# Optimization experiments

Measured on AMD Instinct MI355X. Metric: run time of the kernel, lower is better.

Reference implementation:

```python
import jax, jax.numpy as jnp
import numpy as np

N = 50000
E = 800000
DIM = 256
H = 8
HD = DIM // H


def setup_inputs() -> dict:
    key = jax.random.key(0)
    ks = jax.random.split(key, 8)
    s = 0.02
    return {
        "x": jax.random.normal(ks[0], (N, DIM), jnp.float32),
        "src": jax.random.randint(ks[1], (E,), 0, N, jnp.int32),
        "dst": jax.random.randint(ks[2], (E,), 0, N, jnp.int32),
        "Wqkv": jax.random.normal(ks[3], (DIM, 3 * DIM), jnp.float32) * s,
        "bqkv": jnp.zeros((3 * DIM,), jnp.float32),
        "Wout": jax.random.normal(ks[4], (DIM, DIM), jnp.float32) * s,
        "bout": jnp.zeros((DIM,), jnp.float32),
        "W1": jax.random.normal(ks[5], (2 * DIM, DIM), jnpp := jnp.float32) * s,
        "b1": jnp.zeros((DIM,), jnp.float32),
        "W2": jax.random.normal(ks[6], (DIM, DIM), jnp.float32) * s,
        "b2": jnp.zeros((DIM,), jnp.float32),
    }


def reference(x, src, dst, Wqkv, bqkv, Wout, bout, W1, b1, W2, b2):
    n = x.shape[0]
    scale = 1.0 / np.sqrt(HD).astype(np.float32)
    # QKV projection; torch reshapes [N, 3*dim] -> [N, H, 3*hd] then splits per head
    qkv = (x @ Wqkv + bqkv).reshape(n, H, 3 * HD)
    q, k, v = qkv[..., :HD], qkv[..., HD:2 * HD], qkv[..., 2 * HD:]
    # per-edge attention scores: key at src dotted with query at dst -> [E, H]
    scores = jnp.einsum('ehd,ehd->eh', k[src], q[dst]) * scale
    # edge softmax grouped by destination node
    m = jax.ops.segment_max(scores, dst, num_segments=n)  # [N, H]
    p = jnp.exp(scores - m[dst])
    denom = jax.ops.segment_sum(p, dst, num_segments=n)  # [N, H]
    probs = p / denom[dst]
    # weighted scatter-sum aggregation of source values -> [N, H, HD]
    agg = jax.ops.segment_sum(v[src] * probs[..., None], dst, num_segments=n)
    agg = agg.reshape(n, DIM) @ Wout + bout
    # feed-forward over concat([x, aggregated])
    h = jnp.concatenate([x, agg], axis=1)
    h = jax.nn.gelu(h @ W1 + b1, approximate=False)
    return h @ W2 + b2
```

## Files before the change

kernel.cpp:

```cpp
#include <hip/hip_runtime.h>
#include <hip/hip_bf16.h>
#include <math.h>

#define NDIM 256
#define HDIM 32
#define SCB 512

typedef __attribute__((ext_vector_type(8))) short bf16x8;
typedef __attribute__((ext_vector_type(4))) float f32x4;
typedef __attribute__((ext_vector_type(2))) float f32x2;
typedef unsigned long long ull;

__device__ inline float bf2f(unsigned short u) {
  union { unsigned int i; float f; } c; c.i = ((unsigned int)u) << 16; return c.f;
}
__device__ inline unsigned short f2bf(float f) {
  union { float f; unsigned int i; } c; c.f = f;
  unsigned int x = c.i;
  unsigned int lsb = (x >> 16) & 1u;
  x += 0x7fffu + lsb;
  return (unsigned short)(x >> 16);
}
__device__ inline float4 ldbf4(const unsigned short* p) {
  ull raw = *(const ull*)p;
  float4 f;
  f.x = bf2f((unsigned short)(raw));
  f.y = bf2f((unsigned short)(raw >> 16));
  f.z = bf2f((unsigned short)(raw >> 32));
  f.w = bf2f((unsigned short)(raw >> 48));
  return f;
}
__device__ inline void stbf4(unsigned short* p, float4 v) {
  ull raw = (ull)f2bf(v.x) | ((ull)f2bf(v.y) << 16)
          | ((ull)f2bf(v.z) << 32) | ((ull)f2bf(v.w) << 48);
  *(ull*)p = raw;
}
__device__ inline ull pk4_bf16(float v0, float v1, float v2, float v3) {
  return (ull)f2bf(v0) | ((ull)f2bf(v1) << 16) | ((ull)f2bf(v2) << 32) | ((ull)f2bf(v3) << 48);
}

__device__ inline unsigned char f2e4m3(float v) {
#if __has_builtin(__builtin_amdgcn_cvt_pk_fp8_f32)
  return (unsigned char)(__builtin_amdgcn_cvt_pk_fp8_f32(v, v, 0, false) & 0xff);
#else
  union { float f; unsigned int u; } c; c.f = v;
  unsigned char s = (unsigned char)((c.u >> 24) & 0x80);
  float a = fabsf(v);
  if (!(a < 448.f)) return (unsigned char)(s | 0x7e);
  if (a < 0.0009765625f) return s;
  int e = (int)((c.u >> 23) & 0xff) - 127;
  if (e < -6) {
    int q = (int)rintf(ldexpf(a, 9));
    if (q >= 8) return (unsigned char)(s | 0x08);
    return (unsigned char)(s | q);
  }
  int q = (int)rintf(ldexpf(a, 3 - e));
  if (q == 16) { e++; q = 8; }
  if (e > 8) return (unsigned char)(s | 0x7e);
  return (unsigned char)(s | ((e + 7) << 3) | (q - 8));
#endif
}
__device__ inline unsigned int pk4_e4m3(float v0, float v1, float v2, float v3) {
#if __has_builtin(__builtin_amdgcn_cvt_pk_fp8_f32)
  int w = __builtin_amdgcn_cvt_pk_fp8_f32(v0, v1, 0, false);
  w = __builtin_amdgcn_cvt_pk_fp8_f32(v2, v3, w, true);
  return (unsigned int)w;
#else
  return (unsigned int)f2e4m3(v0) | ((unsigned int)f2e4m3(v1) << 8)
       | ((unsigned int)f2e4m3(v2) << 16) | ((unsigned int)f2e4m3(v3) << 24);
#endif
}
template<bool HI>
__device__ inline f32x2 e4m3pk(unsigned int w) {
#if __has_builtin(__builtin_amdgcn_cvt_pk_f32_fp8)
  return __builtin_amdgcn_cvt_pk_f32_fp8((int)w, HI);
#else
  unsigned int h = HI ? (w >> 16) : w;
  f32x2 r;
  #pragma unroll
  for (int j = 0; j < 2; ++j) {
    unsigned char b = (unsigned char)(h >> (8 * j));
    int e = (b >> 3) & 0xf, mm = b & 7;
    float val = e ? ldexpf((float)(8 + mm), e - 10) : ldexpf((float)mm, -9);
    r[j] = (b & 0x80) ? -val : val;
  }
  return r;
#endif
}

__global__ void fuse0_k(
    const float* __restrict__ x, unsigned short* __restrict__ xb, int n8, int nbx,
    const float* __restrict__ Wqkv, unsigned short* __restrict__ wqkvt,
    const float* __restrict__ W1, unsigned short* __restrict__ wf,
    const float* __restrict__ W2, unsigned short* __restrict__ w2t,
    const float* __restrict__ Wout, const float* __restrict__ bout,
    const float* __restrict__ b1, float* __restrict__ bc, int nbw,
    const int* __restrict__ dst, int* __restrict__ deg, int E)
{
  int b = blockIdx.x;
  int tid = threadIdx.x;
  if (b < nbx) {
    int i = b * 256 + tid;
    if (i < n8) {
      const float* p = x + (size_t)i * 8;
      float4 a = *(const float4*)p;
      float4 bv = *(const float4*)(p + 4);
      ull lo = (ull)f2bf(a.x) | ((ull)f2bf(a.y) << 16) | ((ull)f2bf(a.z) << 32) | ((ull)f2bf(a.w) << 48);
      ull hi = (ull)f2bf(bv.x) | ((ull)f2bf(bv.y) << 16) | ((ull)f2bf(bv.z) << 32) | ((ull)f2bf(bv.w) << 48);
      ull* d = (ull*)(xb + (size_t)i * 8);
      d[0] = lo; d[1] = hi;
    }
    return;
  }
  b -= nbx;
  if (b < nbw) {
    int idx = b * 256 + tid;
    if (idx < 196608) {
      int j = idx >> 8, k = idx & 255;
      int seg = j >> 8, jj = j & 255;
      int h = jj >> 5, t = jj & 31;
      int orig = h * 96 + seg * 32 + t;
      wqkvt[(size_t)j * 256 + k] = f2bf(Wqkv[(size_t)k * 768 + orig]);
    } else if (idx < 262144) {
      int i2 = idx - 196608;
      int n = i2 >> 8, k = i2 & 255;
      wf[(size_t)n * 512 + k] = f2bf(W1[(size_t)k * 256 + n]);
    } else if (idx < 327680) {
      int i3 = idx - 262144;
      int n = i3 >> 8, k = i3 & 255;
      w2t[(size_t)n * 256 + k] = f2bf(W2[(size_t)k * 256 + n]);
    } else if (idx < 393216) {
      int i4 = idx - 327680;
      int a = i4 >> 8, n = i4 & 255;
      float s = 0.f;
      #pragma unroll 4
      for (int j = 0; j < 256; ++j)
        s += Wout[(size_t)a * 256 + j] * W1[(size_t)(256 + j) * 256 + n];
      wf[(size_t)n * 512 + 256 + a] = f2bf(s);
    } else if (idx < 393472) {
      int n = idx - 393216;
      float s = b1[n];
      for (int j = 0; j < 256; ++j)
        s += bout[j] * W1[(size_t)(256 + j) * 256 + n];
      bc[n] = s;
    }
    return;
  }
  b -= nbw;
  int e = b * 256 + tid;
  if (e < E) atomicAdd(&deg[dst[e]], 1);
}

__global__ __launch_bounds__(SCB) void bsum_k(const int* __restrict__ deg, int* __restrict__ bsum, int n) {
  int tid = threadIdx.x;
  int i = blockIdx.x * SCB + tid;
  int v = (i < n) ? deg[i] : 0;
  #pragma unroll
  for (int d = 1; d < 64; d <<= 1) v += __shfl_xor(v, d);
  __shared__ int wsum[8];
  if ((tid & 63) == 0) wsum[tid >> 6] = v;
  __syncthreads();
  if (tid == 0) {
    int s = 0;
    #pragma unroll
    for (int j = 0; j < 8; ++j) s += wsum[j];
    bsum[blockIdx.x] = s;
  }
}

__global__ __launch_bounds__(128) void bscan_k(int* __restrict__ bsum, int nb) {
  __shared__ int tmp[128];
  int tid = threadIdx.x;
  int v = (tid < nb) ? bsum[tid] : 0;
  tmp[tid] = v;
  __syncthreads();
  for (int d = 1; d < 128; d <<= 1) {
    int t = (tid >= d) ? tmp[tid - d] : 0;
    __syncthreads();
    tmp[tid] += t;
    __syncthreads();
  }
  if (tid < nb) bsum[tid] = tmp[tid];
}

__global__ __launch_bounds__(SCB) void offs_k(const int* __restrict__ deg, const int* __restrict__ bsum,
                                              int* __restrict__ offs, int* __restrict__ cursor, int n) {
  int tid = threadIdx.x, lane = tid & 63, wid = tid >> 6;
  int b = blockIdx.x;
  int i = b * SCB + tid;
  int v = (i < n) ? deg[i] : 0;
  int incl = v;
  #pragma unroll
  for (int d = 1; d < 64; d <<= 1) { int t = __shfl_up(incl, d); if (lane >= d) incl += t; }
  __shared__ int wsum[8];
  if (lane == 63) wsum[wid] = incl;
  __syncthreads();
  if (tid < 8) {
    int s = wsum[tid];
    #pragma unroll
    for (int d = 1; d < 8; d <<= 1) { int t = __shfl_up(s, d); if (tid >= d) s += t; }
    wsum[tid] = s;
  }
  __syncthreads();
  int base = (b > 0 ? bsum[b - 1] : 0) + (wid > 0 ? wsum[wid - 1] : 0);
  if (i < n) {
    int val = base + incl - v;
    offs[i] = val;
    cursor[i] = val;
  }
  if (i == n - 1) offs[n] = base + incl;
}

__global__ __launch_bounds__(256) void attn_k(
    const unsigned short* Q,
    const unsigned char* __restrict__ K8,
    const unsigned char* __restrict__ V8,
    const int* __restrict__ offs,
    const int* __restrict__ ssrc,
    unsigned short* agg, int N)
{
  int n = blockIdx.x * 4 + (threadIdx.x >> 6);
  if (n >= N) return;
  int lane = threadIdx.x & 63;
  int col = lane << 2;
  const float scale = 0.17677669529663689f;
  float4 q4 = ldbf4(Q + (size_t)n * NDIM + col);
  q4.x *= scale; q4.y *= scale; q4.z *= scale; q4.w *= scale;
  int e0 = offs[n], e1 = offs[n + 1];
  float den = 0.f;
  float ax = 0.f, ay = 0.f, az = 0.f, aw = 0.f;
  int e = e0;
  for (; e + 8 <= e1; e += 8) {
    unsigned int kw[8], vw[8];
    #pragma unroll
    for (int j = 0; j < 8; ++j) {
      int s = ssrc[e + j];
      kw[j] = *(const unsigned int*)(K8 + (size_t)s * NDIM + col);
      vw[j] = *(const unsigned int*)(V8 + (size_t)s * NDIM + col);
    }
    float d[8];
    #pragma unroll
    for (int j = 0; j < 8; ++j) {
      f32x2 k01 = e4m3pk<false>(kw[j]);
      f32x2 k23 = e4m3pk<true>(kw[j]);
      d[j] = q4.x * k01[0] + q4.y * k01[1] + q4.z * k23[0] + q4.w * k23[1];
    }
    #pragma unroll
    for (int j = 0; j < 8; ++j) {
      d[j] += __shfl_xor(d[j], 1);
      d[j] += __shfl_xor(d[j], 2);
      d[j] += __shfl_xor(d[j], 4);
    }
    #pragma unroll
    for (int j = 0; j < 8; ++j) {
      float p = __expf(d[j]);
      den += p;
      f32x2 v01 = e4m3pk<false>(vw[j]);
      f32x2 v23 = e4m3pk<true>(vw[j]);
      ax += p * v01[0]; ay += p * v01[1];
      az += p * v23[0]; aw += p * v23[1];
    }
  }
  for (; e + 4 <= e1; e += 4) {
    unsigned int kw[4], vw[4];
    #pragma unroll
    for (int j = 0; j < 4; ++j) {
      int s = ssrc[e + j];
      kw[j] = *(const unsigned int*)(K8 + (size_t)s * NDIM + col);
      vw[j] = *(const unsigned int*)(V8 + (size_t)s * NDIM + col);
    }
    float d[4];
    #pragma unroll
    for (int j = 0; j < 4; ++j) {
      f32x2 k01 = e4m3pk<false>(kw[j]);
      f32x2 k23 = e4m3pk<true>(kw[j]);
      d[j] = q4.x * k01[0] + q4.y * k01[1] + q4.z * k23[0] + q4.w * k23[1];
    }
    #pragma unroll
    for (int j = 0; j < 4; ++j) {
      d[j] += __shfl_xor(d[j], 1);
      d[j] += __shfl_xor(d[j], 2);
      d[j] += __shfl_xor(d[j], 4);
    }
    #pragma unroll
    for (int j = 0; j < 4; ++j) {
      float p = __expf(d[j]);
      den += p;
      f32x2 v01 = e4m3pk<false>(vw[j]);
      f32x2 v23 = e4m3pk<true>(vw[j]);
      ax += p * v01[0]; ay += p * v01[1];
      az += p * v23[0]; aw += p * v23[1];
    }
  }
  for (; e < e1; ++e) {
    int s = ssrc[e];
    unsigned int kw = *(const unsigned int*)(K8 + (size_t)s * NDIM + col);
    unsigned int vw = *(const unsigned int*)(V8 + (size_t)s * NDIM + col);
    f32x2 k01 = e4m3pk<false>(kw);
    f32x2 k23 = e4m3pk<true>(kw);
    float d = q4.x * k01[0] + q4.y * k01[1] + q4.z * k23[0] + q4.w * k23[1];
    d += __shfl_xor(d, 1);
    d += __shfl_xor(d, 2);
    d += __shfl_xor(d, 4);
    float p = __expf(d);
    den += p;
    f32x2 v01 = e4m3pk<false>(vw);
    f32x2 v23 = e4m3pk<true>(vw);
    ax += p * v01[0]; ay += p * v01[1];
    az += p * v23[0]; aw += p * v23[1];
  }
  float inv = (den > 0.f) ? 1.f / den : 0.f;
  stbf4(agg + (size_t)n * NDIM + col, make_float4(ax * inv, ay * inv, az * inv, aw * inv));
}

__global__ __launch_bounds__(256, 4) void sqkv_k(
    const int* __restrict__ src, const int* __restrict__ dstv,
    int* __restrict__ cursor, int* __restrict__ ssrc, int E, int nsc,
    const unsigned short* __restrict__ A1, const unsigned short* __restrict__ Wt,
    const float* __restrict__ bias,
    unsigned short* __restrict__ Oq, unsigned char* __restrict__ Ok, unsigned char* __restrict__ Ov,
    int M)
{
  __shared__ char smem[32768];
  if (blockIdx.x < nsc) {
    int e = blockIdx.x * 256 + threadIdx.x;
    if (e < E) {
      int p = atomicAdd(&cursor[dstv[e]], 1);
      ssrc[p] = src[e];
    }
    return;
  }
  unsigned short* As = (unsigned short*)smem;
  unsigned short* Bs = (unsigned short*)(smem + 16384);
  const int tid = threadIdx.x;
  const int lane = tid & 63;
  const int wid = tid >> 6;

  const int nwg = gridDim.x - nsc;
  const int bid = blockIdx.x - nsc;
  const int q8 = nwg >> 3, r8 = nwg & 7;
  const int xcd = bid & 7, idx8 = bid >> 3;
  const int swz = (xcd < r8 ? xcd * (q8 + 1) : r8 * (q8 + 1) + (xcd - r8) * q8) + idx8;
  const int nct = 6;
  const int bmt = swz / nct;
  const int bnt = swz - bmt * nct;
  const int bm = bmt * 128;
  const int bn = bnt * 128;

  const int wr = (wid >> 1) << 6;
  const int wc = (wid & 1) << 6;
  const int l15 = lane & 15, lhi = lane >> 4;
  const int srow = lane >> 3;
  const int ssl = (((lane & 7) ^ (lane >> 3)) << 3);

  f32x4 acc[4][4];
  #pragma unroll
  for (int i = 0; i < 4; ++i)
    #pragma unroll
    for (int j = 0; j < 4; ++j) acc[i][j] = (f32x4){0.f, 0.f, 0.f, 0.f};

  for (int k0 = 0; k0 < 256; k0 += 64) {
    #pragma unroll
    for (int t = 0; t < 4; ++t) {
      int qi = wid * 4 + t;
      const unsigned short* ga = A1 + (size_t)(bm + qi * 8 + srow) * 256 + k0 + ssl;
      __builtin_amdgcn_global_load_lds(
          (const __attribute__((address_space(1))) void*)ga,
          (__attribute__((address_space(3))) void*)&As[qi * 512], 16, 0, 0);
      const unsigned short* gb = Wt + (size_t)(bn + qi * 8 + srow) * 256 + k0 + ssl;
      __builtin_amdgcn_global_load_lds(
          (const __attribute__((address_space(1))) void*)gb,
          (__attribute__((address_space(3))) void*)&Bs[qi * 512], 16, 0, 0);
    }
    __syncthreads();
    #pragma unroll
    for (int kk = 0; kk < 64; kk += 32) {
      bf16x8 af[4], bfr[4];
      #pragma unroll
      for (int mi = 0; mi < 4; ++mi) {
        int rA = wr + mi * 16 + l15;
        af[mi] = *(const bf16x8*)&As[rA * 64 + ((((kk >> 3) + lhi) ^ (rA & 7)) << 3)];
      }
      #pragma unroll
      for (int ni = 0; ni < 4; ++ni) {
        int rB = wc + ni * 16 + l15;
        bfr[ni] = *(const bf16x8*)&Bs[rB * 64 + ((((kk >> 3) + lhi) ^ (rB & 7)) << 3)];
      }
      #pragma unroll
      for (int mi = 0; mi < 4; ++mi)
        #pragma unroll
        for (int ni = 0; ni < 4; ++ni)
          acc[mi][ni] = __builtin_amdgcn_mfma_f32_16x16x32_bf16(bfr[ni], af[mi], acc[mi][ni], 0, 0, 0);
    }
    __syncthreads();
  }

  const int seg = (bn + wc) >> 8;
  const int jjbase = (bn + wc) & 255;
  if (seg == 0) {
    unsigned short* slab = (unsigned short*)(smem + wid * 8192);
    #pragma unroll
    for (int ni = 0; ni < 4; ++ni) {
      int cl = ni * 16 + (lhi << 2);
      int jj = jjbase + cl;
      float4 bb = *(const float4*)&bias[(jj >> 5) * 96 + (jj & 31)];
      #pragma unroll
      for (int mi = 0; mi < 4; ++mi) {
        int rl = mi * 16 + l15;
        *(ull*)&slab[rl * 64 + cl] = pk4_bf16(
            acc[mi][ni][0] + bb.x, acc[mi][ni][1] + bb.y,
            acc[mi][ni][2] + bb.z, acc[mi][ni][3] + bb.w);
      }
    }
    asm volatile("s_waitcnt lgkmcnt(0)" ::: "memory");
    __builtin_amdgcn_sched_barrier(0);
    int rl0 = lane >> 3, coff = (lane & 7) << 3;
    #pragma unroll
    for (int t = 0; t < 8; ++t) {
      int rl = t * 8 + rl0;
      int gr = bm + wr + rl;
      if (gr < M)
        *(float4*)&Oq[(size_t)gr * NDIM + jjbase + coff] = *(float4*)&slab[rl * 64 + coff];
    }
  } else {
    unsigned char* slab8 = (unsigned char*)(smem + wid * 8192);
    unsigned char* dstp = (seg == 1) ? Ok : Ov;
    #pragma unroll
    for (int ni = 0; ni < 4; ++ni) {
      int cl = ni * 16 + (lhi << 2);
      int jj = jjbase + cl;
      float4 bb = *(const float4*)&bias[(jj >> 5) * 96 + seg * 32 + (jj & 31)];
      #pragma unroll
      for (int mi = 0; mi < 4; ++mi) {
        int rl = mi * 16 + l15;
        *(unsigned int*)&slab8[rl * 64 + cl] = pk4_e4m3(
            acc[mi][ni][0] + bb.x, acc[mi][ni][1] + bb.y,
            acc[mi][ni][2] + bb.z, acc[mi][ni][3] + bb.w);
      }
    }
    asm volatile("s_waitcnt lgkmcnt(0)" ::: "memory");
    __builtin_amdgcn_sched_barrier(0);
    int rl0 = lane >> 2, coff = (lane & 3) << 4;
    #pragma unroll
    for (int t = 0; t < 4; ++t) {
      int rl = t * 16 + rl0;
      int gr = bm + wr + rl;
      if (gr < M)
        *(float4*)&dstp[(size_t)gr * NDIM + jjbase + coff] = *(float4*)&slab8[rl * 64 + coff];
    }
  }
}

template<int EPI>
__global__ __launch_bounds__(256, 4) void mgemm_k(
    const unsigned short* __restrict__ A1, const unsigned short* __restrict__ A2,
    const unsigned short* __restrict__ Wt, const float* __restrict__ bias,
    float* __restrict__ Cf, unsigned short* __restrict__ Cb,
    int M, int K1, int K, int Ncol, int ldb, int nct)
{
  __shared__ char smem[32768];
  unsigned short* As = (unsigned short*)smem;
  unsigned short* Bs = (unsigned short*)(smem + 16384);
  const int tid = threadIdx.x;
  const int lane = tid & 63;
  const int wid = tid >> 6;

  const int nwg = gridDim.x;
  const int q8 = nwg >> 3, r8 = nwg & 7;
  const int xcd = blockIdx.x & 7, idx8 = blockIdx.x >> 3;
  const int swz = (xcd < r8 ? xcd * (q8 + 1) : r8 * (q8 + 1) + (xcd - r8) * q8) + idx8;
  const int bmt = swz / nct;
  const int bnt = swz - bmt * nct;
  const int bm = bmt * 128;
  const int bn = bnt * 128;

  const int wr = (wid >> 1) << 6;
  const int wc = (wid & 1) << 6;
  const int l15 = lane & 15, lhi = lane >> 4;
  const int srow = lane >> 3;
  const int ssl = (((lane & 7) ^ (lane >> 3)) << 3);

  f32x4 acc[4][4];
  #pragma unroll
  for (int i = 0; i < 4; ++i)
    #pragma unroll
    for (int j = 0; j < 4; ++j) acc[i][j] = (f32x4){0.f, 0.f, 0.f, 0.f};

  for (int k0 = 0; k0 < K; k0 += 64) {
    const unsigned short* Ab;
    int ks;
    if (k0 < K1) { Ab = A1; ks = k0; } else { Ab = A2; ks = k0 - K1; }
    #pragma unroll
    for (int t = 0; t < 4; ++t) {
      int qi = wid * 4 + t;
      const unsigned short* ga = Ab + (size_t)(bm + qi * 8 + srow) * 256 + ks + ssl;
      __builtin_amdgcn_global_load_lds(
          (const __attribute__((address_space(1))) void*)ga,
          (__attribute__((address_space(3))) void*)&As[qi * 512], 16, 0, 0);
      const unsigned short* gb = Wt + (size_t)(bn + qi * 8 + srow) * ldb + k0 + ssl;
      __builtin_amdgcn_global_load_lds(
          (const __attribute__((address_space(1))) void*)gb,
          (__attribute__((address_space(3))) void*)&Bs[qi * 512], 16, 0, 0);
    }
    __syncthreads();
    #pragma unroll
    for (int kk = 0; kk < 64; kk += 32) {
      bf16x8 af[4], bfr[4];
      #pragma unroll
      for (int mi = 0; mi < 4; ++mi) {
        int rA = wr + mi * 16 + l15;
        af[mi] = *(const bf16x8*)&As[rA * 64 + ((((kk >> 3) + lhi) ^ (rA & 7)) << 3)];
      }
      #pragma unroll
      for (int ni = 0; ni < 4; ++ni) {
        int rB = wc + ni * 16 + l15;
        bfr[ni] = *(const bf16x8*)&Bs[rB * 64 + ((((kk >> 3) + lhi) ^ (rB & 7)) << 3)];
      }
      #pragma unroll
      for (int mi = 0; mi < 4; ++mi)
        #pragma unroll
        for (int ni = 0; ni < 4; ++ni)
          acc[mi][ni] = __builtin_amdgcn_mfma_f32_16x16x32_bf16(bfr[ni], af[mi], acc[mi][ni], 0, 0, 0);
    }
    __syncthreads();
  }

  if (EPI == 0) {
    float* slabf = (float*)(smem + wid * 8192);
    #pragma unroll
    for (int half = 0; half < 2; ++half) {
      #pragma unroll
      for (int nj = 0; nj < 2; ++nj) {
        int ni = half * 2 + nj;
        int cl = nj * 16 + (lhi << 2);
        float4 bb = *(const float4*)&bias[bn + wc + half * 32 + cl];
        #pragma unroll
        for (int mi = 0; mi < 4; ++mi) {
          int rl = mi * 16 + l15;
          *(float4*)&slabf[rl * 32 + cl] = make_float4(
              acc[mi][ni][0] + bb.x, acc[mi][ni][1] + bb.y,
              acc[mi][ni][2] + bb.z, acc[mi][ni][3] + bb.w);
        }
      }
      asm volatile("s_waitcnt lgkmcnt(0)" ::: "memory");
      __builtin_amdgcn_sched_barrier(0);
      int rl0 = lane >> 3, coff = (lane & 7) << 2;
      #pragma unroll
      for (int t = 0; t < 8; ++t) {
        int rl = t * 8 + rl0;
        int gr = bm + wr + rl;
        if (gr < M)
          *(float4*)&Cf[(size_t)gr * Ncol + bn + wc + half * 32 + coff] =
              *(float4*)&slabf[rl * 32 + coff];
      }
      if (half == 0) {
        asm volatile("s_waitcnt lgkmcnt(0)" ::: "memory");
        __builtin_amdgcn_sched_barrier(0);
      }
    }
  } else {
    unsigned short* slab = (unsigned short*)(smem + wid * 8192);
    #pragma unroll
    for (int ni = 0; ni < 4; ++ni) {
      int cl = ni * 16 + (lhi << 2);
      float4 bb = *(const float4*)&bias[bn + wc + cl];
      #pragma unroll
      for (int mi = 0; mi < 4; ++mi) {
        int rl = mi * 16 + l15;
        float v0 = acc[mi][ni][0] + bb.x;
        float v1 = acc[mi][ni][1] + bb.y;
        float v2 = acc[mi][ni][2] + bb.z;
        float v3 = acc[mi][ni][3] + bb.w;
        v0 = 0.5f * v0 * (1.0f + erff(v0 * 0.70710678118654752f));
        v1 = 0.5f * v1 * (1.0f + erff(v1 * 0.70710678118654752f));
        v2 = 0.5f * v2 * (1.0f + erff(v2 * 0.70710678118654752f));
        v3 = 0.5f * v3 * (1.0f + erff(v3 * 0.70710678118654752f));
        *(ull*)&slab[rl * 64 + cl] = pk4_bf16(v0, v1, v2, v3);
      }
    }
    asm volatile("s_waitcnt lgkmcnt(0)" ::: "memory");
    __builtin_amdgcn_sched_barrier(0);
    int rl0 = lane >> 3, coff = (lane & 7) << 3;
    #pragma unroll
    for (int t = 0; t < 8; ++t) {
      int rl = t * 8 + rl0;
      int gr = bm + wr + rl;
      if (gr < M)
        *(float4*)&Cb[(size_t)gr * Ncol + bn + wc + coff] = *(float4*)&slab[rl * 64 + coff];
    }
  }
}

extern "C" void kernel_launch(void* const* d_in, const int* in_sizes, int n_in,
                              void* d_out, int out_size, void* d_ws, size_t ws_size,
                              hipStream_t stream) {
  (void)n_in; (void)out_size; (void)ws_size;
  const float* x    = (const float*)d_in[0];
  const int*   src  = (const int*)d_in[1];
  const int*   dst  = (const int*)d_in[2];
  const float* Wqkv = (const float*)d_in[3];
  const float* bqkv = (const float*)d_in[4];
  const float* Wout = (const float*)d_in[5];
  const float* bout = (const float*)d_in[6];
  const float* W1   = (const float*)d_in[7];
  const float* b1   = (const float*)d_in[8];
  const float* W2   = (const float*)d_in[9];
  const float* b2   = (const float*)d_in[10];
  float* out = (float*)d_out;

  const int N = in_sizes[0] / NDIM;
  const int E = in_sizes[1];
  const int Mp = (N + 127) & ~127;
  const int nb = (N + SCB - 1) / SCB;

  char* ws = (char*)d_ws;
  size_t off = 0;
  auto alloc = [&](size_t bytes) -> char* {
    char* p = ws + off;
    off += (bytes + 255) & ~(size_t)255;
    return p;
  };
  unsigned short* xb   = (unsigned short*)alloc((size_t)Mp * NDIM * 2);
  unsigned short* Q    = (unsigned short*)alloc((size_t)Mp * NDIM * 2);
  unsigned short* Kb   = (unsigned short*)alloc((size_t)Mp * NDIM * 2);
  unsigned short* Vb   = (unsigned short*)alloc((size_t)Mp * NDIM * 2);
  unsigned short* wqkvt = (unsigned short*)alloc((size_t)768 * 256 * 2);
  unsigned short* wft   = (unsigned short*)alloc((size_t)256 * 512 * 2);
  unsigned short* w2t   = (unsigned short*)alloc((size_t)256 * 256 * 2);
  float*          bc    = (float*)alloc(256 * 4);
  int* deg    = (int*)alloc((size_t)N * 4);
  int* offs   = (int*)alloc((size_t)(N + 1) * 4);
  int* cursor = (int*)alloc((size_t)N * 4);
  int* ssrc   = (int*)alloc((size_t)E * 4);
  int* bsum   = (int*)alloc((size_t)nb * 4);

  unsigned char* K8 = (unsigned char*)Kb;
  unsigned char* V8 = (unsigned char*)Vb;
  unsigned short* agg = Q;
  unsigned short* h1  = Kb;

  const int n8  = N * NDIM / 8;
  const int nbx = (n8 + 255) / 256;
  const int nbw = (393472 + 255) / 256;
  const int nsc = (E + 255) / 256;
  const int mt  = Mp / 128;

  hipMemsetAsync(deg, 0, (size_t)N * 4, stream);

  fuse0_k<<<nbx + nbw + nsc, 256, 0, stream>>>(
      x, xb, n8, nbx, Wqkv, wqkvt, W1, wft, W2, w2t, Wout, bout, b1, bc, nbw,
      dst, deg, E);

  bsum_k<<<nb, SCB, 0, stream>>>(deg, bsum, N);
  bscan_k<<<1, 128, 0, stream>>>(bsum, nb);
  offs_k<<<nb, SCB, 0, stream>>>(deg, bsum, offs, cursor, N);

  sqkv_k<<<nsc + mt * 6, 256, 0, stream>>>(
      src, dst, cursor, ssrc, E, nsc,
      xb, wqkvt, bqkv, Q, K8, V8, N);

  attn_k<<<(N + 3) / 4, 256, 0, stream>>>(Q, K8, V8, offs, ssrc, agg, N);

  mgemm_k<2><<<mt * 2, 256, 0, stream>>>(
      xb, agg, wft, bc, nullptr, h1, N, 256, 512, 256, 512, 2);

  mgemm_k<0><<<mt * 2, 256, 0, stream>>>(
      h1, nullptr, w2t, b2, out, nullptr, N, 256, 256, 256, 256, 2);
}
```

Measured before the change: 265.8 us.

## Record edge ranks in degree pass, atomic-free CSR scatter; swizzle epilogue LDS slabs

The degree-count atomics now keep their returned rank per edge. A separate non-atomic scatter kernel then places each source index at offs[dst]+rank, which removes the second round of cursor atomics that was fused into the QKV GEMM launch. The QKV GEMM becomes a standalone kernel. All GEMM epilogue LDS staging slabs now use XOR-swizzled addresses to cut bank conflicts. In exchange it adds an E-sized rank buffer, an extra kernel launch, and loses the overlap between the scatter and the GEMM.

```diff
diff --git a/kernel.cpp b/kernel.cpp
--- a/kernel.cpp
+++ b/kernel.cpp
@@ -95,7 +95,7 @@
     const float* __restrict__ W2, unsigned short* __restrict__ w2t,
     const float* __restrict__ Wout, const float* __restrict__ bout,
     const float* __restrict__ b1, float* __restrict__ bc, int nbw,
-    const int* __restrict__ dst, int* __restrict__ deg, int E)
+    const int* __restrict__ dst, int* __restrict__ deg, int* __restrict__ erank, int E)
 {
   int b = blockIdx.x;
   int tid = threadIdx.x;
@@ -148,7 +148,10 @@
   }
   b -= nbw;
   int e = b * 256 + tid;
-  if (e < E) atomicAdd(&deg[dst[e]], 1);
+  if (e < E) {
+    int r = atomicAdd(&deg[dst[e]], 1);
+    erank[e] = r;
+  }
 }
 
 __global__ __launch_bounds__(SCB) void bsum_k(const int* __restrict__ deg, int* __restrict__ bsum, int n) {
@@ -184,7 +187,7 @@
 }
 
 __global__ __launch_bounds__(SCB) void offs_k(const int* __restrict__ deg, const int* __restrict__ bsum,
-                                              int* __restrict__ offs, int* __restrict__ cursor, int n) {
+                                              int* __restrict__ offs, int n) {
   int tid = threadIdx.x, lane = tid & 63, wid = tid >> 6;
   int b = blockIdx.x;
   int i = b * SCB + tid;
@@ -203,12 +206,15 @@
   }
   __syncthreads();
   int base = (b > 0 ? bsum[b - 1] : 0) + (wid > 0 ? wsum[wid - 1] : 0);
-  if (i < n) {
-    int val = base + incl - v;
-    offs[i] = val;
-    cursor[i] = val;
-  }
+  if (i < n) offs[i] = base + incl - v;
   if (i == n - 1) offs[n] = base + incl;
+}
+
+__global__ void scatter2_k(const int* __restrict__ src, const int* __restrict__ dstv,
+                           const int* __restrict__ offs, const int* __restrict__ erank,
+                           int* __restrict__ ssrc, int E) {
+  int e = blockIdx.x * 256 + threadIdx.x;
+  if (e < E) ssrc[offs[dstv[e]] + erank[e]] = src[e];
 }
 
 __global__ __launch_bounds__(256) void attn_k(
@@ -313,33 +319,22 @@
   stbf4(agg + (size_t)n * NDIM + col, make_float4(ax * inv, ay * inv, az * inv, aw * inv));
 }
 
-__global__ __launch_bounds__(256, 4) void sqkv_k(
-    const int* __restrict__ src, const int* __restrict__ dstv,
-    int* __restrict__ cursor, int* __restrict__ ssrc, int E, int nsc,
+__global__ __launch_bounds__(256, 4) void qkv_k(
     const unsigned short* __restrict__ A1, const unsigned short* __restrict__ Wt,
     const float* __restrict__ bias,
     unsigned short* __restrict__ Oq, unsigned char* __restrict__ Ok, unsigned char* __restrict__ Ov,
     int M)
 {
   __shared__ char smem[32768];
-  if (blockIdx.x < nsc) {
-    int e = blockIdx.x * 256 + threadIdx.x;
-    if (e < E) {
-      int p = atomicAdd(&cursor[dstv[e]], 1);
-      ssrc[p] = src[e];
-    }
-    return;
-  }
   unsigned short* As = (unsigned short*)smem;
   unsigned short* Bs = (unsigned short*)(smem + 16384);
   const int tid = threadIdx.x;
   const int lane = tid & 63;
   const int wid = tid >> 6;
 
-  const int nwg = gridDim.x - nsc;
-  const int bid = blockIdx.x - nsc;
+  const int nwg = gridDim.x;
   const int q8 = nwg >> 3, r8 = nwg & 7;
-  const int xcd = bid & 7, idx8 = bid >> 3;
+  const int xcd = blockIdx.x & 7, idx8 = blockIdx.x >> 3;
   const int swz = (xcd < r8 ? xcd * (q8 + 1) : r8 * (q8 + 1) + (xcd - r8) * q8) + idx8;
   const int nct = 6;
   const int bmt = swz / nct;
@@ -397,8 +392,8 @@
 
   const int seg = (bn + wc) >> 8;
   const int jjbase = (bn + wc) & 255;
+  char* slabB = smem + wid * 8192;
   if (seg == 0) {
-    unsigned short* slab = (unsigned short*)(smem + wid * 8192);
     #pragma unroll
     for (int ni = 0; ni < 4; ++ni) {
       int cl = ni * 16 + (lhi << 2);
@@ -407,23 +402,23 @@
       #pragma unroll
       for (int mi = 0; mi < 4; ++mi) {
         int rl = mi * 16 + l15;
-        *(ull*)&slab[rl * 64 + cl] = pk4_bf16(
+        *(ull*)&slabB[rl * 128 + ((cl * 2) ^ ((rl & 7) << 4))] = pk4_bf16(
             acc[mi][ni][0] + bb.x, acc[mi][ni][1] + bb.y,
             acc[mi][ni][2] + bb.z, acc[mi][ni][3] + bb.w);
       }
     }
     asm volatile("s_waitcnt lgkmcnt(0)" ::: "memory");
     __builtin_amdgcn_sched_barrier(0);
-    int rl0 = lane >> 3, coff = (lane & 7) << 3;
+    int rl0 = lane >> 3, co = (lane & 7) << 4;
     #pragma unroll
     for (int t = 0; t < 8; ++t) {
       int rl = t * 8 + rl0;
       int gr = bm + wr + rl;
       if (gr < M)
-        *(float4*)&Oq[(size_t)gr * NDIM + jjbase + coff] = *(float4*)&slab[rl * 64 + coff];
+        *(float4*)&Oq[(size_t)gr * NDIM + jjbase + (co >> 1)] =
+            *(float4*)&slabB[rl * 128 + (co ^ ((rl & 7) << 4))];
     }
   } else {
-    unsigned char* slab8 = (unsigned char*)(smem + wid * 8192);
     unsigned char* dstp = (seg == 1) ? Ok : Ov;
     #pragma unroll
     for (int ni = 0; ni < 4; ++ni) {
@@ -433,20 +428,21 @@
       #pragma unroll
       for (int mi = 0; mi < 4; ++mi) {
         int rl = mi * 16 + l15;
-        *(unsigned int*)&slab8[rl * 64 + cl] = pk4_e4m3(
+        *(unsigned int*)&slabB[rl * 64 + (cl ^ ((rl & 3) << 4))] = pk4_e4m3(
             acc[mi][ni][0] + bb.x, acc[mi][ni][1] + bb.y,
             acc[mi][ni][2] + bb.z, acc[mi][ni][3] + bb.w);
       }
     }
     asm volatile("s_waitcnt lgkmcnt(0)" ::: "memory");
     __builtin_amdgcn_sched_barrier(0);
-    int rl0 = lane >> 2, coff = (lane & 3) << 4;
+    int rl0 = lane >> 2, co = (lane & 3) << 4;
     #pragma unroll
     for (int t = 0; t < 4; ++t) {
       int rl = t * 16 + rl0;
       int gr = bm + wr + rl;
       if (gr < M)
-        *(float4*)&dstp[(size_t)gr * NDIM + jjbase + coff] = *(float4*)&slab8[rl * 64 + coff];
+        *(float4*)&dstp[(size_t)gr * NDIM + jjbase + co] =
+            *(float4*)&slabB[rl * 64 + (co ^ ((rl & 3) << 4))];
     }
   }
 }
@@ -525,8 +521,8 @@
     __syncthreads();
   }
 
+  char* slabB = smem + wid * 8192;
   if (EPI == 0) {
-    float* slabf = (float*)(smem + wid * 8192);
     #pragma unroll
     for (int half = 0; half < 2; ++half) {
       #pragma unroll
@@ -537,21 +533,21 @@
         #pragma unroll
         for (int mi = 0; mi < 4; ++mi) {
           int rl = mi * 16 + l15;
-          *(float4*)&slabf[rl * 32 + cl] = make_float4(
+          *(float4*)&slabB[rl * 128 + ((cl * 4) ^ ((rl & 7) << 4))] = make_float4(
               acc[mi][ni][0] + bb.x, acc[mi][ni][1] + bb.y,
               acc[mi][ni][2] + bb.z, acc[mi][ni][3] + bb.w);
         }
       }
       asm volatile("s_waitcnt lgkmcnt(0)" ::: "memory");
       __builtin_amdgcn_sched_barrier(0);
-      int rl0 = lane >> 3, coff = (lane & 7) << 2;
+      int rl0 = lane >> 3, co = (lane & 7) << 4;
       #pragma unroll
       for (int t = 0; t < 8; ++t) {
         int rl = t * 8 + rl0;
         int gr = bm + wr + rl;
         if (gr < M)
-          *(float4*)&Cf[(size_t)gr * Ncol + bn + wc + half * 32 + coff] =
-              *(float4*)&slabf[rl * 32 + coff];
+          *(float4*)&Cf[(size_t)gr * Ncol + bn + wc + half * 32 + (co >> 2)] =
+              *(float4*)&slabB[rl * 128 + (co ^ ((rl & 7) << 4))];
       }
       if (half == 0) {
         asm volatile("s_waitcnt lgkmcnt(0)" ::: "memory");
@@ -559,7 +555,6 @@
       }
     }
   } else {
-    unsigned short* slab = (unsigned short*)(smem + wid * 8192);
     #pragma unroll
     for (int ni = 0; ni < 4; ++ni) {
       int cl = ni * 16 + (lhi << 2);
@@ -575,18 +570,19 @@
         v1 = 0.5f * v1 * (1.0f + erff(v1 * 0.70710678118654752f));
         v2 = 0.5f * v2 * (1.0f + erff(v2 * 0.70710678118654752f));
         v3 = 0.5f * v3 * (1.0f + erff(v3 * 0.70710678118654752f));
-        *(ull*)&slab[rl * 64 + cl] = pk4_bf16(v0, v1, v2, v3);
+        *(ull*)&slabB[rl * 128 + ((cl * 2) ^ ((rl & 7) << 4))] = pk4_bf16(v0, v1, v2, v3);
       }
     }
     asm volatile("s_waitcnt lgkmcnt(0)" ::: "memory");
     __builtin_amdgcn_sched_barrier(0);
-    int rl0 = lane >> 3, coff = (lane & 7) << 3;
+    int rl0 = lane >> 3, co = (lane & 7) << 4;
     #pragma unroll
     for (int t = 0; t < 8; ++t) {
       int rl = t * 8 + rl0;
       int gr = bm + wr + rl;
       if (gr < M)
-        *(float4*)&Cb[(size_t)gr * Ncol + bn + wc + coff] = *(float4*)&slab[rl * 64 + coff];
+        *(float4*)&Cb[(size_t)gr * Ncol + bn + wc + (co >> 1)] =
+            *(float4*)&slabB[rl * 128 + (co ^ ((rl & 7) << 4))];
     }
   }
 }
@@ -630,7 +626,7 @@
   float*          bc    = (float*)alloc(256 * 4);
   int* deg    = (int*)alloc((size_t)N * 4);
   int* offs   = (int*)alloc((size_t)(N + 1) * 4);
-  int* cursor = (int*)alloc((size_t)N * 4);
+  int* erank  = (int*)alloc((size_t)E * 4);
   int* ssrc   = (int*)alloc((size_t)E * 4);
   int* bsum   = (int*)alloc((size_t)nb * 4);
 
@@ -649,15 +645,15 @@
 
   fuse0_k<<<nbx + nbw + nsc, 256, 0, stream>>>(
       x, xb, n8, nbx, Wqkv, wqkvt, W1, wft, W2, w2t, Wout, bout, b1, bc, nbw,
-      dst, deg, E);
+      dst, deg, erank, E);
 
   bsum_k<<<nb, SCB, 0, stream>>>(deg, bsum, N);
   bscan_k<<<1, 128, 0, stream>>>(bsum, nb);
-  offs_k<<<nb, SCB, 0, stream>>>(deg, bsum, offs, cursor, N);
-
-  sqkv_k<<<nsc + mt * 6, 256, 0, stream>>>(
-      src, dst, cursor, ssrc, E, nsc,
-      xb, wqkvt, bqkv, Q, K8, V8, N);
+  offs_k<<<nb, SCB, 0, stream>>>(deg, bsum, offs, N);
+
+  scatter2_k<<<nsc, 256, 0, stream>>>(src, dst, offs, erank, ssrc, E);
+
+  qkv_k<<<mt * 6, 256, 0, stream>>>(xb, wqkvt, bqkv, Q, K8, V8, N);
 
   attn_k<<<(N + 3) / 4, 256, 0, stream>>>(Q, K8, V8, offs, ssrc, agg, N);
 
```

Result: faster. 220.8 us (-16.9%).
